# Kernel tuning notes

Measured on AMD Instinct MI355X. Metric: run time of the kernel, lower is better.

Reference implementation:

```python
import jax, jax.numpy as jnp
import numpy as np

EMBED = 64
N, T, F = 8, 64, 512

def setup_inputs() -> dict:
    key = jax.random.key(0)
    ks = jax.random.split(key, 8)
    shp = (N, T, F, EMBED)
    s = 1.0 / np.sqrt(EMBED)
    return {
        "value": jax.random.normal(ks[0], shp, jnp.float32),
        "key": jax.random.normal(ks[1], shp, jnp.float32),
        "query": jax.random.normal(ks[2], shp, jnp.float32),
        "Wv": jax.random.normal(ks[3], (EMBED, EMBED), jnp.float32) * s,
        "Wk": jax.random.normal(ks[4], (EMBED, EMBED), jnp.float32) * s,
        "Wq": jax.random.normal(ks[5], (EMBED, EMBED), jnp.float32) * s,
        "Wo": jax.random.normal(ks[6], (EMBED, EMBED), jnp.float32) * s,
        "bo": jax.random.normal(ks[7], (EMBED,), jnp.float32) * 0.01,
    }

def reference(value, key, query, Wv, Wk, Wq, Wo, bo):
    # nn.Linear applies y = x @ W.T (no bias for v/k/q)
    values = jnp.einsum('ntfe,de->ntfd', value, Wv)
    keys = jnp.einsum('ntfe,de->ntfd', key, Wk)
    queries = jnp.einsum('ntfe,de->ntfd', query, Wq)
    # contract over time t; attend over freq (q,k); embed e is a batch dim
    energy = jnp.einsum('ntqe,ntke->neqk', queries, keys)  # [N,e,Fq,Fk]
    scale = jnp.asarray(EMBED, energy.dtype) ** 0.5
    attention = jax.nn.softmax(energy / scale, axis=3)
    out = jnp.einsum('neqk,ntke->ntqe', attention, values)  # [N,T,Fq,e]
    out = jnp.einsum('ntqe,de->ntqd', out, Wo) + bo
    return out
```

## Files before the change

### kernel.cpp

```cpp
#include <hip/hip_runtime.h>
#include <hip/hip_bf16.h>

#define T_ 64
#define F_ 512
#define E_ 64
#define N_ 8
#define PROJ_ELEMS ((size_t)N_ * E_ * F_ * T_)
#define NSLAB ((size_t)E_ * F_ * T_)

typedef short bf16x8 __attribute__((ext_vector_type(8)));
typedef unsigned short u16x8 __attribute__((ext_vector_type(8)));
typedef unsigned short u16x4 __attribute__((ext_vector_type(4)));
typedef float f32x4 __attribute__((ext_vector_type(4)));

static __device__ __forceinline__ f32x4 mfma_bf16(bf16x8 a, bf16x8 b, f32x4 c) {
  return __builtin_amdgcn_mfma_f32_16x16x32_bf16(a, b, c, 0, 0, 0);
}

static __device__ __forceinline__ unsigned short f2bf(float x) {
  union { float f; unsigned u; } v; v.f = x;
  unsigned r = v.u + 0x7fffu + ((v.u >> 16) & 1u);
  return (unsigned short)(r >> 16);
}
static __device__ __forceinline__ float bf2f(unsigned short s) {
  union { unsigned u; float f; } v; v.u = ((unsigned)s) << 16;
  return v.f;
}

static __device__ __forceinline__ unsigned pack_bf16(float lo, float hi) {
#if __has_builtin(__builtin_amdgcn_cvt_pk_bf16_f32)
  typedef __bf16 bf16x2_t __attribute__((ext_vector_type(2)));
  union { bf16x2_t v; unsigned u; } c;
  c.v = __builtin_amdgcn_cvt_pk_bf16_f32(lo, hi);
  return c.u;
#else
  return ((unsigned)f2bf(lo)) | (((unsigned)f2bf(hi)) << 16);
#endif
}

static __device__ __forceinline__ bool detect_f32(const unsigned short* w) {
  bool m = false;
#pragma unroll
  for (int i = 0; i < 64; ++i) m |= ((unsigned)(w[i] & 0x7F80u) >= 0x4000u);
  return m;
}

__global__ __launch_bounds__(256) void proj_kernel(
    const void* __restrict__ Xv, const void* __restrict__ Wv,
    unsigned short* __restrict__ out, int n_base) {
  __shared__ unsigned short chunk[8 * 64 * 72];
  const int nb = blockIdx.y;
  const int na = nb + n_base;
  const int f0 = blockIdx.x * 8;
  const int tid = (int)threadIdx.x;
  const int lane = tid & 63, wv = tid >> 6;
  const int lr = lane & 15, quad = lane >> 4;
  const bool f32m = detect_f32((const unsigned short*)Wv);

  bf16x8 wf[4][2];
  if (!f32m) {
    const unsigned short* W = (const unsigned short*)Wv;
#pragma unroll
    for (int dt = 0; dt < 4; ++dt)
#pragma unroll
      for (int h = 0; h < 2; ++h)
        wf[dt][h] = *(const bf16x8*)(W + (dt * 16 + lr) * 64 + h * 32 + quad * 8);
  } else {
    const float* W = (const float*)Wv;
#pragma unroll
    for (int dt = 0; dt < 4; ++dt)
#pragma unroll
      for (int h = 0; h < 2; ++h) {
        const float* p = W + (dt * 16 + lr) * 64 + h * 32 + quad * 8;
        float4 x0 = *(const float4*)p;
        float4 x1 = *(const float4*)(p + 4);
        bf16x8 t;
        t[0] = (short)f2bf(x0.x); t[1] = (short)f2bf(x0.y);
        t[2] = (short)f2bf(x0.z); t[3] = (short)f2bf(x0.w);
        t[4] = (short)f2bf(x1.x); t[5] = (short)f2bf(x1.y);
        t[6] = (short)f2bf(x1.z); t[7] = (short)f2bf(x1.w);
        wf[dt][h] = t;
      }
  }

  for (int tile = wv; tile < 128; tile += 4) {
    const int tc = tile >> 5;
    const int f  = (tile >> 2) & 7;
    const int dt = tile & 3;
    const size_t xoff =
        ((size_t)((na * T_ + tc * 16 + lr) * F_ + f0 + f)) * E_ + quad * 8;
    bf16x8 a0, a1;
    if (!f32m) {
      const unsigned short* xp = (const unsigned short*)Xv + xoff;
      a0 = *(const bf16x8*)xp;
      a1 = *(const bf16x8*)(xp + 32);
    } else {
      const float* xp = (const float*)Xv + xoff;
      float4 x0 = *(const float4*)(xp + 0);
      float4 x1 = *(const float4*)(xp + 4);
      float4 x2 = *(const float4*)(xp + 32);
      float4 x3 = *(const float4*)(xp + 36);
      bf16x8 t0, t1;
      t0[0] = (short)f2bf(x0.x); t0[1] = (short)f2bf(x0.y);
      t0[2] = (short)f2bf(x0.z); t0[3] = (short)f2bf(x0.w);
      t0[4] = (short)f2bf(x1.x); t0[5] = (short)f2bf(x1.y);
      t0[6] = (short)f2bf(x1.z); t0[7] = (short)f2bf(x1.w);
      t1[0] = (short)f2bf(x2.x); t1[1] = (short)f2bf(x2.y);
      t1[2] = (short)f2bf(x2.z); t1[3] = (short)f2bf(x2.w);
      t1[4] = (short)f2bf(x3.x); t1[5] = (short)f2bf(x3.y);
      t1[6] = (short)f2bf(x3.z); t1[7] = (short)f2bf(x3.w);
      a0 = t0; a1 = t1;
    }
    f32x4 acc = {0.f, 0.f, 0.f, 0.f};
    acc = mfma_bf16(a0, wf[dt][0], acc);
    acc = mfma_bf16(a1, wf[dt][1], acc);
    const int d = dt * 16 + lr;
    const int tb = tc * 16 + quad * 4;
    u16x4 pk;
    pk[0] = f2bf(acc[0]); pk[1] = f2bf(acc[1]);
    pk[2] = f2bf(acc[2]); pk[3] = f2bf(acc[3]);
    *(u16x4*)&chunk[(f * 64 + d) * 72 + tb] = pk;
  }
  __syncthreads();
#pragma unroll
  for (int it = 0; it < 16; ++it) {
    const int slot = it * 256 + tid;
    const int row = slot >> 3;
    const int part = slot & 7;
    const int d = row >> 3;
    const int f = row & 7;
    uint4 v2 = *(const uint4*)&chunk[(f * 64 + d) * 72 + part * 8];
    *(uint4*)(out + ((size_t)((nb * E_ + d) * F_ + f0 + f)) * T_ + part * 8) = v2;
  }
}

__global__ __launch_bounds__(512, 4) void attn_kernel(
    unsigned short* __restrict__ Vp,
    const unsigned short* __restrict__ Kp,
    const unsigned short* __restrict__ Qp, int n_base) {
  __shared__ unsigned short Vlds[T_ * 520];
  __shared__ unsigned short Plds[8 * 16 * 36];
  const int e = blockIdx.x, nb = blockIdx.y;
  const int na = nb + n_base;
  const size_t base = ((size_t)(na * E_ + e)) * (size_t)(F_ * T_);
  const unsigned short* Vb = Vp + base;
  const unsigned short* Kb = Kp + base;
  const unsigned short* Qb = Qp + ((size_t)(nb * E_ + e)) * (size_t)(F_ * T_);
  unsigned short* Ob = Vp + base;
  const int tid = (int)threadIdx.x;

#pragma unroll
  for (int it = 0; it < 8; ++it) {
    int slot = it * 512 + tid;
    int t = slot & 63, kg = slot >> 6;
    u16x8 tv;
#pragma unroll
    for (int j = 0; j < 8; ++j) tv[j] = Vb[(kg * 8 + j) * 64 + t];
    *(u16x8*)&Vlds[t * 520 + kg * 8] = tv;
  }
  __syncthreads();

  const int lane = tid & 63, wv = tid >> 6;
  const int lr = lane & 15, quad = lane >> 4;
  unsigned short* Pl = Plds + wv * (16 * 36);
  const float cexp = 0.18033688011112042f;

#pragma unroll
  for (int iter = 0; iter < 2; ++iter) {
    const int q0 = (wv + iter * 8) * 32;
    bf16x8 qf[2][2];
#pragma unroll
    for (int qt = 0; qt < 2; ++qt) {
      const unsigned short* qp = Qb + (q0 + qt * 16 + lr) * 64 + quad * 8;
      qf[qt][0] = *(const bf16x8*)qp;
      qf[qt][1] = *(const bf16x8*)(qp + 32);
    }
    f32x4 o[2][4];
#pragma unroll
    for (int qt = 0; qt < 2; ++qt)
#pragma unroll
      for (int tt = 0; tt < 4; ++tt) o[qt][tt] = (f32x4){0.f, 0.f, 0.f, 0.f};
    float l0 = 0.f, l1 = 0.f;

#pragma unroll 1
    for (int kc = 0; kc < 16; ++kc) {
      f32x4 s[2][2];
#pragma unroll
      for (int h = 0; h < 2; ++h) {
        const unsigned short* kp = Kb + (kc * 32 + h * 16 + lr) * 64 + quad * 8;
        bf16x8 a0 = *(const bf16x8*)kp;
        bf16x8 a1 = *(const bf16x8*)(kp + 32);
#pragma unroll
        for (int qt = 0; qt < 2; ++qt) {
          f32x4 acc = {0.f, 0.f, 0.f, 0.f};
          acc = mfma_bf16(a0, qf[qt][0], acc);
          acc = mfma_bf16(a1, qf[qt][1], acc);
          s[qt][h] = acc;
        }
      }
#pragma unroll
      for (int qt = 0; qt < 2; ++qt) {
        float lacc = 0.f;
#pragma unroll
        for (int h = 0; h < 2; ++h) {
          float p0 = __builtin_amdgcn_exp2f(s[qt][h][0] * cexp);
          float p1 = __builtin_amdgcn_exp2f(s[qt][h][1] * cexp);
          float p2 = __builtin_amdgcn_exp2f(s[qt][h][2] * cexp);
          float p3 = __builtin_amdgcn_exp2f(s[qt][h][3] * cexp);
          lacc += (p0 + p1) + (p2 + p3);
          uint2 w;
          w.x = pack_bf16(p0, p1);
          w.y = pack_bf16(p2, p3);
          *(uint2*)&Pl[lr * 36 + h * 16 + quad * 4] = w;
        }
        if (qt == 0) l0 += lacc; else l1 += lacc;
        bf16x8 pf = *(const bf16x8*)&Pl[lr * 36 + quad * 8];
#pragma unroll
        for (int tt = 0; tt < 4; ++tt) {
          bf16x8 vf = *(const bf16x8*)&Vlds[(tt * 16 + lr) * 520 + kc * 32 + quad * 8];
          o[qt][tt] = mfma_bf16(vf, pf, o[qt][tt]);
        }
      }
    }
    l0 += __shfl_xor(l0, 16); l0 += __shfl_xor(l0, 32);
    l1 += __shfl_xor(l1, 16); l1 += __shfl_xor(l1, 32);
    const float r0 = __builtin_amdgcn_rcpf(l0);
    const float r1 = __builtin_amdgcn_rcpf(l1);
#pragma unroll
    for (int qt = 0; qt < 2; ++qt) {
      const float rv = qt ? r1 : r0;
#pragma unroll
      for (int tt = 0; tt < 4; ++tt) {
        u16x4 pk;
        pk[0] = f2bf(o[qt][tt][0] * rv);
        pk[1] = f2bf(o[qt][tt][1] * rv);
        pk[2] = f2bf(o[qt][tt][2] * rv);
        pk[3] = f2bf(o[qt][tt][3] * rv);
        *(u16x4*)(Ob + (q0 + qt * 16 + lr) * 64 + tt * 16 + quad * 4) = pk;
      }
    }
  }
}

__global__ __launch_bounds__(256) void outproj_kernel(
    const void* __restrict__ Wov, const void* __restrict__ bov,
    const unsigned short* __restrict__ Obuf, void* __restrict__ outv) {
  const int tid = (int)threadIdx.x;
  const int lane = tid & 63, wv = tid >> 6;
  const int lr = lane & 15, quad = lane >> 4;
  const int unit = (int)blockIdx.x * 4 + wv;
  const int n = unit >> 9, q = unit & 511;
  const bool f32m = detect_f32((const unsigned short*)Wov);

  bf16x8 a[4][2];
  float bias[4][4];
  if (!f32m) {
    const unsigned short* Wo = (const unsigned short*)Wov;
    const unsigned short* bo = (const unsigned short*)bov;
#pragma unroll
    for (int dt = 0; dt < 4; ++dt)
#pragma unroll
      for (int h = 0; h < 2; ++h)
        a[dt][h] = *(const bf16x8*)(Wo + (dt * 16 + lr) * 64 + h * 32 + quad * 8);
#pragma unroll
    for (int dt = 0; dt < 4; ++dt)
#pragma unroll
      for (int r = 0; r < 4; ++r)
        bias[dt][r] = bf2f(bo[dt * 16 + quad * 4 + r]);
  } else {
    const float* Wo = (const float*)Wov;
    const float* bo = (const float*)bov;
#pragma unroll
    for (int dt = 0; dt < 4; ++dt)
#pragma unroll
      for (int h = 0; h < 2; ++h) {
        const float* p = Wo + (dt * 16 + lr) * 64 + h * 32 + quad * 8;
        float4 x0 = *(const float4*)p;
        float4 x1 = *(const float4*)(p + 4);
        bf16x8 t;
        t[0] = (short)f2bf(x0.x); t[1] = (short)f2bf(x0.y);
        t[2] = (short)f2bf(x0.z); t[3] = (short)f2bf(x0.w);
        t[4] = (short)f2bf(x1.x); t[5] = (short)f2bf(x1.y);
        t[6] = (short)f2bf(x1.z); t[7] = (short)f2bf(x1.w);
        a[dt][h] = t;
      }
#pragma unroll
    for (int dt = 0; dt < 4; ++dt)
#pragma unroll
      for (int r = 0; r < 4; ++r)
        bias[dt][r] = bo[dt * 16 + quad * 4 + r];
  }

  const unsigned short* ObBase = Obuf + ((size_t)(n * E_) * F_ + q) * T_;
#pragma unroll
  for (int tt = 0; tt < 4; ++tt) {
    bf16x8 b[2];
#pragma unroll
    for (int h = 0; h < 2; ++h) {
      bf16x8 bv;
#pragma unroll
      for (int j = 0; j < 8; ++j) {
        const int ee = h * 32 + quad * 8 + j;
        bv[j] = (short)ObBase[(size_t)ee * (F_ * T_) + tt * 16 + lr];
      }
      b[h] = bv;
    }
#pragma unroll
    for (int dt = 0; dt < 4; ++dt) {
      f32x4 acc = {0.f, 0.f, 0.f, 0.f};
      acc = mfma_bf16(a[dt][0], b[0], acc);
      acc = mfma_bf16(a[dt][1], b[1], acc);
      const size_t o =
          ((size_t)((n * T_ + tt * 16 + lr) * F_ + q)) * E_ + dt * 16 + quad * 4;
      if (!f32m) {
        u16x4 pk;
        pk[0] = f2bf(acc[0] + bias[dt][0]);
        pk[1] = f2bf(acc[1] + bias[dt][1]);
        pk[2] = f2bf(acc[2] + bias[dt][2]);
        pk[3] = f2bf(acc[3] + bias[dt][3]);
        *(u16x4*)((unsigned short*)outv + o) = pk;
      } else {
        float4 w;
        w.x = acc[0] + bias[dt][0];
        w.y = acc[1] + bias[dt][1];
        w.z = acc[2] + bias[dt][2];
        w.w = acc[3] + bias[dt][3];
        *(float4*)((float*)outv + o) = w;
      }
    }
  }
}

extern "C" void kernel_launch(void* const* d_in, const int* in_sizes, int n_in,
                              void* d_out, int out_size, void* d_ws, size_t ws_size,
                              hipStream_t stream) {
  (void)in_sizes; (void)n_in; (void)out_size;
  const void* value = d_in[0];
  const void* key_  = d_in[1];
  const void* query = d_in[2];
  const void* Wv    = d_in[3];
  const void* Wk    = d_in[4];
  const void* Wq    = d_in[5];
  const void* Wo    = d_in[6];
  const void* bo    = d_in[7];

  unsigned short* Vws  = (unsigned short*)d_ws;
  unsigned short* Qbuf = (unsigned short*)d_ws + PROJ_ELEMS;
  unsigned short* Kbuf = (unsigned short*)d_out;

  long spare = (long)ws_size - (long)(PROJ_ELEMS * 2);
  long qn = spare / (long)(NSLAB * 2);
  int nchunk = qn < 1 ? 1 : (qn > 8 ? 8 : (int)qn);

  hipLaunchKernelGGL(proj_kernel, dim3(F_ / 8, N_), dim3(256), 0, stream,
                     value, Wv, Vws, 0);
  hipLaunchKernelGGL(proj_kernel, dim3(F_ / 8, N_), dim3(256), 0, stream,
                     key_, Wk, Kbuf, 0);
  for (int n0 = 0; n0 < N_; n0 += nchunk) {
    int c = (N_ - n0 < nchunk) ? (N_ - n0) : nchunk;
    hipLaunchKernelGGL(proj_kernel, dim3(F_ / 8, c), dim3(256), 0, stream,
                       query, Wq, Qbuf, n0);
    hipLaunchKernelGGL(attn_kernel, dim3(E_, c), dim3(512), 0, stream,
                       Vws, Kbuf, Qbuf, n0);
  }
  hipLaunchKernelGGL(outproj_kernel, dim3(1024), dim3(256), 0, stream,
                     Wo, bo, Vws, d_out);
}
```

Baseline: 385.7 us.

## Merge QKV projections into one launch, retile proj, prefetch K in attention

The three projection launches become one proj_kernel launch with blockIdx.z picking value, key or query when the workspace holds all batches. Each block now covers 4 frequencies instead of 8, so the grid doubles, and each wave reuses its loaded input row across all four output column tiles. In attention, the next K chunk is now prefetched into registers and the V fragments are loaded from LDS before the softmax. This trades extra register pressure for hidden global load latency.

```diff
diff --git a/kernel.cpp b/kernel.cpp
--- a/kernel.cpp
+++ b/kernel.cpp
@@ -45,13 +45,31 @@
   return m;
 }
 
+static __device__ __forceinline__ bf16x8 cvt8(const float* p) {
+  float4 x0 = *(const float4*)p;
+  float4 x1 = *(const float4*)(p + 4);
+  bf16x8 t;
+  t[0] = (short)f2bf(x0.x); t[1] = (short)f2bf(x0.y);
+  t[2] = (short)f2bf(x0.z); t[3] = (short)f2bf(x0.w);
+  t[4] = (short)f2bf(x1.x); t[5] = (short)f2bf(x1.y);
+  t[6] = (short)f2bf(x1.z); t[7] = (short)f2bf(x1.w);
+  return t;
+}
+
 __global__ __launch_bounds__(256) void proj_kernel(
-    const void* __restrict__ Xv, const void* __restrict__ Wv,
-    unsigned short* __restrict__ out, int n_base) {
-  __shared__ unsigned short chunk[8 * 64 * 72];
+    const void* __restrict__ Xv0, const void* __restrict__ Xv1,
+    const void* __restrict__ Xv2, const void* __restrict__ Wv0,
+    const void* __restrict__ Wv1, const void* __restrict__ Wv2,
+    unsigned short* __restrict__ o0, unsigned short* __restrict__ o1,
+    unsigned short* __restrict__ o2, int n_base, int which) {
+  __shared__ unsigned short chunk[4 * 64 * 76];
+  const int p = (which < 0) ? (int)blockIdx.z : which;
+  const void* Xv = (p == 0) ? Xv0 : ((p == 1) ? Xv1 : Xv2);
+  const void* Wv = (p == 0) ? Wv0 : ((p == 1) ? Wv1 : Wv2);
+  unsigned short* out = (p == 0) ? o0 : ((p == 1) ? o1 : o2);
   const int nb = blockIdx.y;
-  const int na = nb + n_base;
-  const int f0 = blockIdx.x * 8;
+  const int na = nb + ((p == 2) ? n_base : 0);
+  const int f0 = blockIdx.x * 4;
   const int tid = (int)threadIdx.x;
   const int lane = tid & 63, wv = tid >> 6;
   const int lr = lane & 15, quad = lane >> 4;
@@ -70,25 +88,14 @@
 #pragma unroll
     for (int dt = 0; dt < 4; ++dt)
 #pragma unroll
-      for (int h = 0; h < 2; ++h) {
-        const float* p = W + (dt * 16 + lr) * 64 + h * 32 + quad * 8;
-        float4 x0 = *(const float4*)p;
-        float4 x1 = *(const float4*)(p + 4);
-        bf16x8 t;
-        t[0] = (short)f2bf(x0.x); t[1] = (short)f2bf(x0.y);
-        t[2] = (short)f2bf(x0.z); t[3] = (short)f2bf(x0.w);
-        t[4] = (short)f2bf(x1.x); t[5] = (short)f2bf(x1.y);
-        t[6] = (short)f2bf(x1.z); t[7] = (short)f2bf(x1.w);
-        wf[dt][h] = t;
-      }
-  }
-
-  for (int tile = wv; tile < 128; tile += 4) {
-    const int tc = tile >> 5;
-    const int f  = (tile >> 2) & 7;
-    const int dt = tile & 3;
+      for (int h = 0; h < 2; ++h)
+        wf[dt][h] = cvt8(W + (dt * 16 + lr) * 64 + h * 32 + quad * 8);
+  }
+
+#pragma unroll
+  for (int f = 0; f < 4; ++f) {
     const size_t xoff =
-        ((size_t)((na * T_ + tc * 16 + lr) * F_ + f0 + f)) * E_ + quad * 8;
+        ((size_t)((na * T_ + wv * 16 + lr) * F_ + f0 + f)) * E_ + quad * 8;
     bf16x8 a0, a1;
     if (!f32m) {
       const unsigned short* xp = (const unsigned short*)Xv + xoff;
@@ -96,40 +103,29 @@
       a1 = *(const bf16x8*)(xp + 32);
     } else {
       const float* xp = (const float*)Xv + xoff;
-      float4 x0 = *(const float4*)(xp + 0);
-      float4 x1 = *(const float4*)(xp + 4);
-      float4 x2 = *(const float4*)(xp + 32);
-      float4 x3 = *(const float4*)(xp + 36);
-      bf16x8 t0, t1;
-      t0[0] = (short)f2bf(x0.x); t0[1] = (short)f2bf(x0.y);
-      t0[2] = (short)f2bf(x0.z); t0[3] = (short)f2bf(x0.w);
-      t0[4] = (short)f2bf(x1.x); t0[5] = (short)f2bf(x1.y);
-      t0[6] = (short)f2bf(x1.z); t0[7] = (short)f2bf(x1.w);
-      t1[0] = (short)f2bf(x2.x); t1[1] = (short)f2bf(x2.y);
-      t1[2] = (short)f2bf(x2.z); t1[3] = (short)f2bf(x2.w);
-      t1[4] = (short)f2bf(x3.x); t1[5] = (short)f2bf(x3.y);
-      t1[6] = (short)f2bf(x3.z); t1[7] = (short)f2bf(x3.w);
-      a0 = t0; a1 = t1;
-    }
-    f32x4 acc = {0.f, 0.f, 0.f, 0.f};
-    acc = mfma_bf16(a0, wf[dt][0], acc);
-    acc = mfma_bf16(a1, wf[dt][1], acc);
-    const int d = dt * 16 + lr;
-    const int tb = tc * 16 + quad * 4;
-    u16x4 pk;
-    pk[0] = f2bf(acc[0]); pk[1] = f2bf(acc[1]);
-    pk[2] = f2bf(acc[2]); pk[3] = f2bf(acc[3]);
-    *(u16x4*)&chunk[(f * 64 + d) * 72 + tb] = pk;
+      a0 = cvt8(xp);
+      a1 = cvt8(xp + 32);
+    }
+#pragma unroll
+    for (int dt = 0; dt < 4; ++dt) {
+      f32x4 acc = {0.f, 0.f, 0.f, 0.f};
+      acc = mfma_bf16(a0, wf[dt][0], acc);
+      acc = mfma_bf16(a1, wf[dt][1], acc);
+      u16x4 pk;
+      pk[0] = f2bf(acc[0]); pk[1] = f2bf(acc[1]);
+      pk[2] = f2bf(acc[2]); pk[3] = f2bf(acc[3]);
+      *(u16x4*)&chunk[(f * 64 + dt * 16 + lr) * 76 + wv * 16 + quad * 4] = pk;
+    }
   }
   __syncthreads();
 #pragma unroll
-  for (int it = 0; it < 16; ++it) {
+  for (int it = 0; it < 8; ++it) {
     const int slot = it * 256 + tid;
     const int row = slot >> 3;
     const int part = slot & 7;
-    const int d = row >> 3;
-    const int f = row & 7;
-    uint4 v2 = *(const uint4*)&chunk[(f * 64 + d) * 72 + part * 8];
+    const int d = row >> 2;
+    const int f = row & 3;
+    uint4 v2 = *(const uint4*)&chunk[(f * 64 + d) * 76 + part * 8];
     *(uint4*)(out + ((size_t)((nb * E_ + d) * F_ + f0 + f)) * T_ + part * 8) = v2;
   }
 }
@@ -182,22 +178,38 @@
       for (int tt = 0; tt < 4; ++tt) o[qt][tt] = (f32x4){0.f, 0.f, 0.f, 0.f};
     float l0 = 0.f, l1 = 0.f;
 
+    bf16x8 ka[2][2];
+#pragma unroll
+    for (int h = 0; h < 2; ++h) {
+      const unsigned short* kp = Kb + (h * 16 + lr) * 64 + quad * 8;
+      ka[h][0] = *(const bf16x8*)kp;
+      ka[h][1] = *(const bf16x8*)(kp + 32);
+    }
+
 #pragma unroll 1
     for (int kc = 0; kc < 16; ++kc) {
+      const int kc1 = (kc + 1) & 15;
+      bf16x8 kn[2][2];
+#pragma unroll
+      for (int h = 0; h < 2; ++h) {
+        const unsigned short* kp = Kb + (kc1 * 32 + h * 16 + lr) * 64 + quad * 8;
+        kn[h][0] = *(const bf16x8*)kp;
+        kn[h][1] = *(const bf16x8*)(kp + 32);
+      }
       f32x4 s[2][2];
 #pragma unroll
-      for (int h = 0; h < 2; ++h) {
-        const unsigned short* kp = Kb + (kc * 32 + h * 16 + lr) * 64 + quad * 8;
-        bf16x8 a0 = *(const bf16x8*)kp;
-        bf16x8 a1 = *(const bf16x8*)(kp + 32);
+      for (int h = 0; h < 2; ++h)
 #pragma unroll
         for (int qt = 0; qt < 2; ++qt) {
           f32x4 acc = {0.f, 0.f, 0.f, 0.f};
-          acc = mfma_bf16(a0, qf[qt][0], acc);
-          acc = mfma_bf16(a1, qf[qt][1], acc);
+          acc = mfma_bf16(ka[h][0], qf[qt][0], acc);
+          acc = mfma_bf16(ka[h][1], qf[qt][1], acc);
           s[qt][h] = acc;
         }
-      }
+      bf16x8 vfr[4];
+#pragma unroll
+      for (int tt = 0; tt < 4; ++tt)
+        vfr[tt] = *(const bf16x8*)&Vlds[(tt * 16 + lr) * 520 + kc * 32 + quad * 8];
 #pragma unroll
       for (int qt = 0; qt < 2; ++qt) {
         float lacc = 0.f;
@@ -216,10 +228,13 @@
         if (qt == 0) l0 += lacc; else l1 += lacc;
         bf16x8 pf = *(const bf16x8*)&Pl[lr * 36 + quad * 8];
 #pragma unroll
-        for (int tt = 0; tt < 4; ++tt) {
-          bf16x8 vf = *(const bf16x8*)&Vlds[(tt * 16 + lr) * 520 + kc * 32 + quad * 8];
-          o[qt][tt] = mfma_bf16(vf, pf, o[qt][tt]);
-        }
+        for (int tt = 0; tt < 4; ++tt)
+          o[qt][tt] = mfma_bf16(vfr[tt], pf, o[qt][tt]);
+      }
+#pragma unroll
+      for (int h = 0; h < 2; ++h) {
+        ka[h][0] = kn[h][0];
+        ka[h][1] = kn[h][1];
       }
     }
     l0 += __shfl_xor(l0, 16); l0 += __shfl_xor(l0, 32);
@@ -273,17 +288,8 @@
 #pragma unroll
     for (int dt = 0; dt < 4; ++dt)
 #pragma unroll
-      for (int h = 0; h < 2; ++h) {
-        const float* p = Wo + (dt * 16 + lr) * 64 + h * 32 + quad * 8;
-        float4 x0 = *(const float4*)p;
-        float4 x1 = *(const float4*)(p + 4);
-        bf16x8 t;
-        t[0] = (short)f2bf(x0.x); t[1] = (short)f2bf(x0.y);
-        t[2] = (short)f2bf(x0.z); t[3] = (short)f2bf(x0.w);
-        t[4] = (short)f2bf(x1.x); t[5] = (short)f2bf(x1.y);
-        t[6] = (short)f2bf(x1.z); t[7] = (short)f2bf(x1.w);
-        a[dt][h] = t;
-      }
+      for (int h = 0; h < 2; ++h)
+        a[dt][h] = cvt8(Wo + (dt * 16 + lr) * 64 + h * 32 + quad * 8);
 #pragma unroll
     for (int dt = 0; dt < 4; ++dt)
 #pragma unroll
@@ -352,16 +358,23 @@
   long qn = spare / (long)(NSLAB * 2);
   int nchunk = qn < 1 ? 1 : (qn > 8 ? 8 : (int)qn);
 
-  hipLaunchKernelGGL(proj_kernel, dim3(F_ / 8, N_), dim3(256), 0, stream,
-                     value, Wv, Vws, 0);
-  hipLaunchKernelGGL(proj_kernel, dim3(F_ / 8, N_), dim3(256), 0, stream,
-                     key_, Wk, Kbuf, 0);
-  for (int n0 = 0; n0 < N_; n0 += nchunk) {
-    int c = (N_ - n0 < nchunk) ? (N_ - n0) : nchunk;
-    hipLaunchKernelGGL(proj_kernel, dim3(F_ / 8, c), dim3(256), 0, stream,
-                       query, Wq, Qbuf, n0);
-    hipLaunchKernelGGL(attn_kernel, dim3(E_, c), dim3(512), 0, stream,
-                       Vws, Kbuf, Qbuf, n0);
+  if (nchunk >= 8) {
+    hipLaunchKernelGGL(proj_kernel, dim3(F_ / 4, N_, 3), dim3(256), 0, stream,
+                       value, key_, query, Wv, Wk, Wq, Vws, Kbuf, Qbuf, 0, -1);
+    hipLaunchKernelGGL(attn_kernel, dim3(E_, N_), dim3(512), 0, stream,
+                       Vws, Kbuf, Qbuf, 0);
+  } else {
+    hipLaunchKernelGGL(proj_kernel, dim3(F_ / 4, N_, 1), dim3(256), 0, stream,
+                       value, key_, query, Wv, Wk, Wq, Vws, Kbuf, Qbuf, 0, 0);
+    hipLaunchKernelGGL(proj_kernel, dim3(F_ / 4, N_, 1), dim3(256), 0, stream,
+                       value, key_, query, Wv, Wk, Wq, Vws, Kbuf, Qbuf, 0, 1);
+    for (int n0 = 0; n0 < N_; n0 += nchunk) {
+      int c = (N_ - n0 < nchunk) ? (N_ - n0) : nchunk;
+      hipLaunchKernelGGL(proj_kernel, dim3(F_ / 4, c, 1), dim3(256), 0, stream,
+                         value, key_, query, Wv, Wk, Wq, Vws, Kbuf, Qbuf, n0, 2);
+      hipLaunchKernelGGL(attn_kernel, dim3(E_, c), dim3(512), 0, stream,
+                         Vws, Kbuf, Qbuf, n0);
+    }
   }
   hipLaunchKernelGGL(outproj_kernel, dim3(1024), dim3(256), 0, stream,
                      Wo, bo, Vws, d_out);
```

After: 330.2 us. -14.4%, faster.
